# Performance work log

Measured on AMD Instinct MI355X. Metric: run time of the kernel, lower is better.

## Reference

```python
import jax, jax.numpy as jnp
import numpy as np

SOS_TOKEN = 1
MAX_LENGTH = 64
VOCAB = 32000
HIDDEN = 1024
BATCH = 32


def setup_inputs() -> dict:
    key = jax.random.key(0)
    ks = jax.random.split(key, 10)
    s = 1.0 / np.sqrt(HIDDEN)
    return {
        "encoder_outputs": jax.random.normal(ks[0], (BATCH, MAX_LENGTH, HIDDEN), dtype=jnp.float32),
        "encoder_hidden": jax.random.normal(ks[1], (1, BATCH, HIDDEN), dtype=jnp.float32),
        "target_tensor": jax.random.randint(ks[2], (BATCH, MAX_LENGTH), 0, VOCAB),
        "embedding": jax.random.normal(ks[3], (VOCAB, HIDDEN), dtype=jnp.float32),
        "W_ih": jax.random.uniform(ks[4], (3 * HIDDEN, HIDDEN), jnp.float32, -s, s),
        "W_hh": jax.random.uniform(ks[5], (3 * HIDDEN, HIDDEN), jnp.float32, -s, s),
        "b_ih": jax.random.uniform(ks[6], (3 * HIDDEN,), jnp.float32, -s, s),
        "b_hh": jax.random.uniform(ks[7], (3 * HIDDEN,), jnp.float32, -s, s),
        "out_W": jax.random.uniform(ks[8], (VOCAB, HIDDEN), jnp.float32, -s, s),
        "out_b": jax.random.uniform(ks[9], (VOCAB,), jnp.float32, -s, s),
    }


def _decode(encoder_hidden, target_tensor, embedding, W_ih, W_hh, b_ih, b_hh, out_W, out_b):
    B = target_tensor.shape[0]
    # teacher forcing: input at step i is SOS (i=0) else target[:, i-1]
    sos = jnp.full((B, 1), SOS_TOKEN, dtype=target_tensor.dtype)
    inputs = jnp.concatenate([sos, target_tensor[:, :-1]], axis=1)  # [B,T]
    x = jax.nn.relu(embedding[inputs])  # [B,T,H]
    # precompute all input-side gate projections in one GEMM: [B,T,3H]
    xg = jnp.einsum("bth,gh->btg", x, W_ih) + b_ih
    h0 = encoder_hidden[0]  # [B,H]

    def step(h, xg_t):
        hg = h @ W_hh.T + b_hh  # [B,3H]
        xr, xz, xn = jnp.split(xg_t, 3, axis=-1)
        hr, hz, hn = jnp.split(hg, 3, axis=-1)
        r = jax.nn.sigmoid(xr + hr)
        z = jax.nn.sigmoid(xz + hz)
        n = jnp.tanh(xn + r * hn)
        h_new = (1.0 - z) * n + z * h
        return h_new, h_new

    h_last, hs = jax.lax.scan(step, h0, jnp.swapaxes(xg, 0, 1))
    hs = jnp.swapaxes(hs, 0, 1)  # [B,T,H]
    logits = jnp.einsum("bth,vh->btv", hs, out_W) + out_b
    log_probs = jax.nn.log_softmax(logits, axis=-1)
    return log_probs, h_last[None]  # hidden shaped [1,B,H] like torch GRU


def reference(encoder_outputs, encoder_hidden, target_tensor, embedding, W_ih, W_hh, b_ih, b_hh, out_W, out_b):
    del encoder_outputs  # only used for batch size in the original
    return _decode(encoder_hidden, target_tensor, embedding, W_ih, W_hh, b_ih, b_hh, out_W, out_b)
```

## Files before the change

### kernel.cpp

```cpp
#include <hip/hip_runtime.h>
#include <hip/hip_bf16.h>

#define B_ 32
#define T_ 64
#define H_ 1024
#define G3 3072
#define V_ 32000
#define M_ 2048
#define NB_SCAN 64

typedef __attribute__((ext_vector_type(8))) short s16x8;
typedef __attribute__((ext_vector_type(4))) float f32x4;
typedef __bf16 bf16x8 __attribute__((ext_vector_type(8)));

__device__ inline unsigned short f2bf(float f) {
    union { float f; unsigned int u; } v; v.f = f;
    unsigned int u = v.u;
    return (unsigned short)((u + 0x7FFFu + ((u >> 16) & 1u)) >> 16);
}

__device__ inline s16x8 load_b128_cc(const void* p) {
    s16x8 r;
    asm volatile("global_load_dwordx4 %0, %1, off sc0 sc1" : "=v"(r) : "v"(p));
    return r;
}
__device__ inline unsigned int load_b32_cc(const void* p) {
    unsigned int r;
    asm volatile("global_load_dword %0, %1, off sc0 sc1" : "=v"(r) : "v"(p));
    return r;
}
__device__ inline void store_b32_cc(void* p, unsigned int v) {
    asm volatile("global_store_dword %0, %1, off sc0 sc1" :: "v"(p), "v"(v) : "memory");
}

__global__ void cast_f32_bf16(const float* __restrict__ src, unsigned short* __restrict__ dst, int n) {
    int i = (blockIdx.x * blockDim.x + threadIdx.x) * 4;
    int stride = gridDim.x * blockDim.x * 4;
    for (; i < n; i += stride) {
        float4 v = *(const float4*)(src + i);
        ushort4 o;
        o.x = f2bf(v.x); o.y = f2bf(v.y); o.z = f2bf(v.z); o.w = f2bf(v.w);
        *(ushort4*)(dst + i) = o;
    }
}

__global__ void embed_relu(const int* __restrict__ target, const float* __restrict__ emb,
                           unsigned short* __restrict__ x) {
    int m = blockIdx.x;
    int b = m >> 6, t = m & 63;
    int tok = (t == 0) ? 1 : target[b * T_ + t - 1];
    const float* row = emb + (size_t)tok * H_;
    int k = threadIdx.x * 4;
    float4 v = *(const float4*)(row + k);
    ushort4 o;
    o.x = f2bf(fmaxf(v.x, 0.f)); o.y = f2bf(fmaxf(v.y, 0.f));
    o.z = f2bf(fmaxf(v.z, 0.f)); o.w = f2bf(fmaxf(v.w, 0.f));
    *(ushort4*)(x + (size_t)m * H_ + k) = o;
}

__global__ void init_h(const float* __restrict__ enc_hidden, unsigned short* __restrict__ hb) {
    int i = blockIdx.x * blockDim.x + threadIdx.x;
    if (i < B_ * H_) hb[i] = f2bf(enc_hidden[i]);
}

__global__ void zero_u32(unsigned int* __restrict__ p, int n) {
    int i = blockIdx.x * blockDim.x + threadIdx.x;
    if (i < n) p[i] = 0;
}

__global__ __launch_bounds__(256) void gemm_bias(
    const unsigned short* __restrict__ A,
    const unsigned short* __restrict__ Bm,
    const float* __restrict__ bias,
    float* __restrict__ C,
    int N, int K)
{
    __shared__ __align__(16) unsigned short As[2 * 4096];
    __shared__ __align__(16) unsigned short Bs[2 * 4096];
    int n0 = blockIdx.x * 128, m0 = blockIdx.y * 128;
    int tid = threadIdx.x;
    int lane = tid & 63, wv = tid >> 6;
    int wr = wv >> 1, wc = wv & 1;

    f32x4 acc[4][4] = {};

    int o0 = wv * 2048 + lane * 16;
    int row0 = o0 >> 6, ib0 = (o0 & 63) >> 1;
    int o1 = o0 + 1024;
    int row1 = o1 >> 6, ib1 = (o1 & 63) >> 1;

    auto stage = [&](int buf, int k0) {
        const unsigned short* ga0 = A + (size_t)(m0 + row0) * K + k0 + ib0;
        const unsigned short* gb0 = Bm + (size_t)(n0 + row0) * K + k0 + ib0;
        const unsigned short* ga1 = A + (size_t)(m0 + row1) * K + k0 + ib1;
        const unsigned short* gb1 = Bm + (size_t)(n0 + row1) * K + k0 + ib1;
        unsigned short* la0 = As + buf * 4096 + wv * 1024;
        unsigned short* lb0 = Bs + buf * 4096 + wv * 1024;
        __builtin_amdgcn_global_load_lds((const __attribute__((address_space(1))) void*)ga0,
                                         (__attribute__((address_space(3))) void*)la0, 16, 0, 0);
        __builtin_amdgcn_global_load_lds((const __attribute__((address_space(1))) void*)gb0,
                                         (__attribute__((address_space(3))) void*)lb0, 16, 0, 0);
        __builtin_amdgcn_global_load_lds((const __attribute__((address_space(1))) void*)ga1,
                                         (__attribute__((address_space(3))) void*)(la0 + 512), 16, 0, 0);
        __builtin_amdgcn_global_load_lds((const __attribute__((address_space(1))) void*)gb1,
                                         (__attribute__((address_space(3))) void*)(lb0 + 512), 16, 0, 0);
    };

    int kq = (lane >> 4) * 8;
    int rA = wr * 64 + (lane & 15);
    int rB = wc * 64 + (lane & 15);

    int NT = K >> 5;
    stage(0, 0);
    __syncthreads();

    int cur = 0;
    for (int t = 0; t < NT; ++t) {
        if (t + 1 < NT) stage(cur ^ 1, (t + 1) << 5);
        const unsigned short* ab = As + cur * 4096;
        const unsigned short* bb = Bs + cur * 4096;
        s16x8 af[4], bf[4];
#pragma unroll
        for (int i = 0; i < 4; ++i) {
            af[i] = *(const s16x8*)(ab + (rA + i * 16) * 32 + kq);
            bf[i] = *(const s16x8*)(bb + (rB + i * 16) * 32 + kq);
        }
#pragma unroll
        for (int mf = 0; mf < 4; ++mf)
#pragma unroll
            for (int nf = 0; nf < 4; ++nf)
                acc[mf][nf] = __builtin_amdgcn_mfma_f32_16x16x32_bf16(
                    __builtin_bit_cast(bf16x8, af[mf]),
                    __builtin_bit_cast(bf16x8, bf[nf]),
                    acc[mf][nf], 0, 0, 0);
        __syncthreads();
        cur ^= 1;
    }

#pragma unroll
    for (int nf = 0; nf < 4; ++nf) {
        int col = n0 + wc * 64 + nf * 16 + (lane & 15);
        float bv = bias[col];
#pragma unroll
        for (int mf = 0; mf < 4; ++mf) {
            int mbase = m0 + wr * 64 + mf * 16 + (lane >> 4) * 4;
#pragma unroll
            for (int r = 0; r < 4; ++r)
                C[(size_t)(mbase + r) * N + col] = acc[mf][nf][r] + bv;
        }
    }
}

__global__ __launch_bounds__(256) void gru_scan(
    const unsigned short* __restrict__ Whhb,
    const float* __restrict__ b_hh,
    const float* __restrict__ enc_hidden,
    const float* __restrict__ xg,
    unsigned short* __restrict__ hb0, unsigned short* __restrict__ hb1,
    float* __restrict__ hfF,
    unsigned short* __restrict__ hs,
    unsigned int* __restrict__ flags)
{
    __shared__ __align__(16) unsigned short ws_[48 * 1024];
    __shared__ __align__(16) f32x4 red[2][3][64];

    int tid = threadIdx.x;
    int lane = tid & 63, wave = tid >> 6;
    int rt = wave >> 1, kh = wave & 1;
    int ct = blockIdx.x;

    for (int idx = tid; idx < 48 * 128; idx += 256) {
        int r = idx >> 7, slot = idx & 127;
        int g = r >> 4, jr = r & 15;
        s16x8 v = *(const s16x8*)(Whhb + (size_t)(g * H_ + ct * 16 + jr) * H_ + slot * 8);
        *(s16x8*)(ws_ + r * 1024 + (slot ^ (r & 7)) * 8) = v;
    }
    __syncthreads();

    int rr = lane & 15, q = lane >> 4;
    int col = ct * 16 + rr;
    int xsw = rr & 7;
    int kbase = kh * 512;
    int sbase = kh * 64 + q;
    float br = b_hh[col], bz = b_hh[H_ + col], bn = b_hh[2 * H_ + col];
    int b0 = rt * 16 + q * 4;

    float hold[4];
    if (kh == 1) {
#pragma unroll
        for (int r = 0; r < 4; ++r) hold[r] = enc_hidden[(b0 + r) * H_ + col];
    }

    for (int t = 0; t < T_; ++t) {
        const unsigned short* hbp = (t & 1) ? hb1 : hb0;
        unsigned short*       hbn = (t & 1) ? hb0 : hb1;

        const unsigned short* ha = hbp + (size_t)(rt * 16 + rr) * H_ + kbase + q * 8;
        s16x8 af[16];
#pragma unroll
        for (int i = 0; i < 16; ++i) af[i] = load_b128_cc(ha + i * 32);

        float xr[4], xz[4], xn[4];
        if (kh == 1) {
#pragma unroll
            for (int r = 0; r < 4; ++r) {
                const float* xrow = xg + ((size_t)(b0 + r) * T_ + t) * G3;
                xr[r] = xrow[col]; xz[r] = xrow[H_ + col]; xn[r] = xrow[2 * H_ + col];
            }
        }

        f32x4 accr, accz, accn;
        if (kh == 1) {
            accr = (f32x4){br, br, br, br};
            accz = (f32x4){bz, bz, bz, bz};
            accn = (f32x4){bn, bn, bn, bn};
        } else {
            accr = (f32x4){0.f, 0.f, 0.f, 0.f};
            accz = accr; accn = accr;
        }

        asm volatile("s_waitcnt vmcnt(0)");
        __builtin_amdgcn_sched_barrier(0);

#pragma unroll
        for (int kk = 0; kk < 16; ++kk) {
            int so = ((sbase + kk * 4) ^ xsw) * 8;
            s16x8 fr = *(const s16x8*)(ws_ + rr * 1024 + so);
            s16x8 fz = *(const s16x8*)(ws_ + (16 + rr) * 1024 + so);
            s16x8 fn = *(const s16x8*)(ws_ + (32 + rr) * 1024 + so);
            bf16x8 a = __builtin_bit_cast(bf16x8, af[kk]);
            accr = __builtin_amdgcn_mfma_f32_16x16x32_bf16(a, __builtin_bit_cast(bf16x8, fr), accr, 0, 0, 0);
            accz = __builtin_amdgcn_mfma_f32_16x16x32_bf16(a, __builtin_bit_cast(bf16x8, fz), accz, 0, 0, 0);
            accn = __builtin_amdgcn_mfma_f32_16x16x32_bf16(a, __builtin_bit_cast(bf16x8, fn), accn, 0, 0, 0);
        }

        if (kh == 0) {
            red[rt][0][lane] = accr; red[rt][1][lane] = accz; red[rt][2][lane] = accn;
        }
        __syncthreads();
        if (kh == 1) {
            accr += red[rt][0][lane]; accz += red[rt][1][lane]; accn += red[rt][2][lane];
            unsigned int hpk[4];
#pragma unroll
            for (int r = 0; r < 4; ++r) {
                float rg = 1.f / (1.f + __expf(-(xr[r] + accr[r])));
                float zg = 1.f / (1.f + __expf(-(xz[r] + accz[r])));
                float ng = tanhf(xn[r] + rg * accn[r]);
                float hnew = (1.f - zg) * ng + zg * hold[r];
                hold[r] = hnew;
                hpk[r] = f2bf(hnew);
            }
#pragma unroll
            for (int r = 0; r < 4; ++r) {
                unsigned int other = __shfl_xor((int)hpk[r], 1);
                if ((rr & 1) == 0) {
                    unsigned int pk = hpk[r] | (other << 16);
                    size_t e = (size_t)(b0 + r) * H_ + col;
                    store_b32_cc(hbn + e, pk);
                    *(unsigned int*)(hs + ((size_t)(b0 + r) * T_ + t) * H_ + col) = pk;
                }
            }
            if (t == T_ - 1) {
#pragma unroll
                for (int r = 0; r < 4; ++r) hfF[(b0 + r) * H_ + col] = hold[r];
            }
            asm volatile("s_waitcnt vmcnt(0)" ::: "memory");
        }

        if (t < T_ - 1) {
            __syncthreads();
            if (tid == 0) store_b32_cc(flags + ct, (unsigned int)(t + 1));
            unsigned int tgt = (unsigned int)(t + 1);
            while (true) {
                unsigned int f = load_b32_cc(flags + lane);
                asm volatile("s_waitcnt vmcnt(0)");
                if (__all(f >= tgt)) break;
                __builtin_amdgcn_s_sleep(1);
            }
            __builtin_amdgcn_sched_barrier(0);
        }
    }
}

__global__ __launch_bounds__(256) void log_softmax_inplace(float* __restrict__ out) {
    int m = blockIdx.x;
    float* row = out + (size_t)m * V_;
    int tid = threadIdx.x;
    __shared__ float sm[4], ss[4];

    float mx = -1e30f, s = 0.f;
    for (int i = tid * 4; i < V_; i += 1024) {
        float4 v = *(const float4*)(row + i);
        float lm = fmaxf(fmaxf(v.x, v.y), fmaxf(v.z, v.w));
        float ns = __expf(v.x - lm) + __expf(v.y - lm) + __expf(v.z - lm) + __expf(v.w - lm);
        if (lm > mx) { s = s * __expf(mx - lm) + ns; mx = lm; }
        else          { s += ns * __expf(lm - mx); }
    }
    for (int o = 32; o > 0; o >>= 1) {
        float om = __shfl_xor(mx, o), os = __shfl_xor(s, o);
        float nm = fmaxf(mx, om);
        s = s * __expf(mx - nm) + os * __expf(om - nm);
        mx = nm;
    }
    int wv = tid >> 6, lane = tid & 63;
    if (lane == 0) { sm[wv] = mx; ss[wv] = s; }
    __syncthreads();
    float fm = fmaxf(fmaxf(sm[0], sm[1]), fmaxf(sm[2], sm[3]));
    float fs = ss[0] * __expf(sm[0] - fm) + ss[1] * __expf(sm[1] - fm)
             + ss[2] * __expf(sm[2] - fm) + ss[3] * __expf(sm[3] - fm);
    float lse = fm + __logf(fs);

    for (int i = tid * 4; i < V_; i += 1024) {
        float4 v = *(const float4*)(row + i);
        v.x -= lse; v.y -= lse; v.z -= lse; v.w -= lse;
        *(float4*)(row + i) = v;
    }
}

__global__ void copy_f32(const float* __restrict__ src, float* __restrict__ dst, int n) {
    int i = blockIdx.x * blockDim.x + threadIdx.x;
    if (i < n) dst[i] = src[i];
}

extern "C" void kernel_launch(void* const* d_in, const int* in_sizes, int n_in,
                              void* d_out, int out_size, void* d_ws, size_t ws_size,
                              hipStream_t stream) {
    const float* enc_hidden = (const float*)d_in[1];
    const int*   target     = (const int*)d_in[2];
    const float* embedding  = (const float*)d_in[3];
    const float* W_ih       = (const float*)d_in[4];
    const float* W_hh       = (const float*)d_in[5];
    const float* b_ih       = (const float*)d_in[6];
    const float* b_hh       = (const float*)d_in[7];
    const float* out_W      = (const float*)d_in[8];
    const float* out_b      = (const float*)d_in[9];
    float* out = (float*)d_out;

    char* ws = (char*)d_ws;
    float*          xg   = (float*)(ws);
    unsigned short* xb   = (unsigned short*)(ws + 25165824);
    unsigned short* hsb  = (unsigned short*)(ws + 29360128);
    unsigned short* wihb = (unsigned short*)(ws + 33554432);
    unsigned short* whhb = (unsigned short*)(ws + 39845888);
    unsigned short* owb  = (unsigned short*)(ws + 46137344);
    float*          hfF  = (float*)(ws + 111673344);
    unsigned short* hb0  = (unsigned short*)(ws + 111804416);
    unsigned short* hb1  = (unsigned short*)(ws + 111869952);
    unsigned int*   flg  = (unsigned int*)(ws + 111935488);

    cast_f32_bf16<<<512, 256, 0, stream>>>(W_ih, wihb, G3 * H_);
    cast_f32_bf16<<<512, 256, 0, stream>>>(W_hh, whhb, G3 * H_);
    cast_f32_bf16<<<2048, 256, 0, stream>>>(out_W, owb, V_ * H_);
    embed_relu<<<M_, 256, 0, stream>>>(target, embedding, xb);
    init_h<<<128, 256, 0, stream>>>(enc_hidden, hb0);
    zero_u32<<<1, 64, 0, stream>>>(flg, 64);

    gemm_bias<<<dim3(G3 / 128, M_ / 128), 256, 0, stream>>>(xb, wihb, b_ih, xg, G3, H_);

    {
        void* args[] = { (void*)&whhb, (void*)&b_hh, (void*)&enc_hidden, (void*)&xg,
                         (void*)&hb0, (void*)&hb1, (void*)&hfF, (void*)&hsb, (void*)&flg };
        hipLaunchCooperativeKernel((const void*)gru_scan, dim3(NB_SCAN), dim3(256), args, 0, stream);
    }

    gemm_bias<<<dim3(V_ / 128, M_ / 128), 256, 0, stream>>>(hsb, owb, out_b, out, V_, H_);
    log_softmax_inplace<<<M_, 256, 0, stream>>>(out);
    copy_f32<<<128, 256, 0, stream>>>(hfF, out + (size_t)M_ * V_, B_ * H_);
}
```

Baseline: 936.9 us.

## Fuse per-tile softmax stats into logits GEMM epilogue and prefetch GRU inputs

The logits GEMM now computes per-row max and sum-exp for each 128-column tile in its epilogue and writes these partials to workspace. A lighter lse_sub kernel combines the 250 partials per row and subtracts the LSE, which removes one full read pass over the 2048x32000 logits. Separately, the GRU scan now loads the next step's xg gate inputs before the inter-block barrier spin, so that load latency overlaps the wait. The cost is extra epilogue shuffles and exp work in the GEMM, and the partials reuse the workspace region that held xb.

```diff
diff --git a/kernel.cpp b/kernel.cpp
--- a/kernel.cpp
+++ b/kernel.cpp
@@ -8,6 +8,7 @@
 #define V_ 32000
 #define M_ 2048
 #define NB_SCAN 64
+#define NTILE_N 250
 
 typedef __attribute__((ext_vector_type(8))) short s16x8;
 typedef __attribute__((ext_vector_type(4))) float f32x4;
@@ -151,6 +152,128 @@
     }
 }
 
+__global__ __launch_bounds__(256) void gemm_logits(
+    const unsigned short* __restrict__ A,
+    const unsigned short* __restrict__ Bm,
+    const float* __restrict__ bias,
+    float* __restrict__ C,
+    float* __restrict__ pmax,
+    float* __restrict__ psum)
+{
+    __shared__ __align__(16) unsigned short As[2 * 4096];
+    __shared__ __align__(16) unsigned short Bs[2 * 4096];
+    __shared__ float spx[2][128], sps[2][128];
+    int n0 = blockIdx.x * 128, m0 = blockIdx.y * 128;
+    int tid = threadIdx.x;
+    int lane = tid & 63, wv = tid >> 6;
+    int wr = wv >> 1, wc = wv & 1;
+
+    f32x4 acc[4][4] = {};
+
+    int o0 = wv * 2048 + lane * 16;
+    int row0 = o0 >> 6, ib0 = (o0 & 63) >> 1;
+    int o1 = o0 + 1024;
+    int row1 = o1 >> 6, ib1 = (o1 & 63) >> 1;
+
+    auto stage = [&](int buf, int k0) {
+        const unsigned short* ga0 = A + (size_t)(m0 + row0) * H_ + k0 + ib0;
+        const unsigned short* gb0 = Bm + (size_t)(n0 + row0) * H_ + k0 + ib0;
+        const unsigned short* ga1 = A + (size_t)(m0 + row1) * H_ + k0 + ib1;
+        const unsigned short* gb1 = Bm + (size_t)(n0 + row1) * H_ + k0 + ib1;
+        unsigned short* la0 = As + buf * 4096 + wv * 1024;
+        unsigned short* lb0 = Bs + buf * 4096 + wv * 1024;
+        __builtin_amdgcn_global_load_lds((const __attribute__((address_space(1))) void*)ga0,
+                                         (__attribute__((address_space(3))) void*)la0, 16, 0, 0);
+        __builtin_amdgcn_global_load_lds((const __attribute__((address_space(1))) void*)gb0,
+                                         (__attribute__((address_space(3))) void*)lb0, 16, 0, 0);
+        __builtin_amdgcn_global_load_lds((const __attribute__((address_space(1))) void*)ga1,
+                                         (__attribute__((address_space(3))) void*)(la0 + 512), 16, 0, 0);
+        __builtin_amdgcn_global_load_lds((const __attribute__((address_space(1))) void*)gb1,
+                                         (__attribute__((address_space(3))) void*)(lb0 + 512), 16, 0, 0);
+    };
+
+    int q = lane >> 4, rr2 = lane & 15;
+    int kq = q * 8;
+    int rA = wr * 64 + rr2;
+    int rB = wc * 64 + rr2;
+
+    stage(0, 0);
+    __syncthreads();
+
+    int cur = 0;
+    for (int t = 0; t < 32; ++t) {
+        if (t + 1 < 32) stage(cur ^ 1, (t + 1) << 5);
+        const unsigned short* ab = As + cur * 4096;
+        const unsigned short* bb = Bs + cur * 4096;
+        s16x8 af[4], bf[4];
+#pragma unroll
+        for (int i = 0; i < 4; ++i) {
+            af[i] = *(const s16x8*)(ab + (rA + i * 16) * 32 + kq);
+            bf[i] = *(const s16x8*)(bb + (rB + i * 16) * 32 + kq);
+        }
+#pragma unroll
+        for (int mf = 0; mf < 4; ++mf)
+#pragma unroll
+            for (int nf = 0; nf < 4; ++nf)
+                acc[mf][nf] = __builtin_amdgcn_mfma_f32_16x16x32_bf16(
+                    __builtin_bit_cast(bf16x8, af[mf]),
+                    __builtin_bit_cast(bf16x8, bf[nf]),
+                    acc[mf][nf], 0, 0, 0);
+        __syncthreads();
+        cur ^= 1;
+    }
+
+    float bv[4];
+#pragma unroll
+    for (int nf = 0; nf < 4; ++nf) bv[nf] = bias[n0 + wc * 64 + nf * 16 + rr2];
+
+#pragma unroll
+    for (int mf = 0; mf < 4; ++mf) {
+#pragma unroll
+        for (int r = 0; r < 4; ++r) {
+            int row_local = wr * 64 + mf * 16 + q * 4 + r;
+            float vmax = -1e30f;
+#pragma unroll
+            for (int nf = 0; nf < 4; ++nf) vmax = fmaxf(vmax, acc[mf][nf][r] + bv[nf]);
+#pragma unroll
+            for (int o = 1; o < 16; o <<= 1) vmax = fmaxf(vmax, __shfl_xor(vmax, o));
+            float vsum = 0.f;
+#pragma unroll
+            for (int nf = 0; nf < 4; ++nf) vsum += __expf(acc[mf][nf][r] + bv[nf] - vmax);
+#pragma unroll
+            for (int o = 1; o < 16; o <<= 1) vsum += __shfl_xor(vsum, o);
+            if (rr2 == 0) { spx[wc][row_local] = vmax; sps[wc][row_local] = vsum; }
+        }
+    }
+
+#pragma unroll
+    for (int nf = 0; nf < 4; ++nf) {
+        int col = n0 + wc * 64 + nf * 16 + rr2;
+#pragma unroll
+        for (int mf = 0; mf < 4; ++mf) {
+            int mbase = m0 + wr * 64 + mf * 16 + q * 4;
+#pragma unroll
+            for (int r = 0; r < 4; ++r)
+                C[(size_t)(mbase + r) * V_ + col] = acc[mf][nf][r] + bv[nf];
+        }
+    }
+
+    __syncthreads();
+    if (wc == 0 && rr2 == 0) {
+#pragma unroll
+        for (int mf = 0; mf < 4; ++mf)
+#pragma unroll
+            for (int r = 0; r < 4; ++r) {
+                int row_local = wr * 64 + mf * 16 + q * 4 + r;
+                float m0v = spx[0][row_local], m1v = spx[1][row_local];
+                float Mv = fmaxf(m0v, m1v);
+                float Sv = sps[0][row_local] * __expf(m0v - Mv) + sps[1][row_local] * __expf(m1v - Mv);
+                pmax[(size_t)(m0 + row_local) * NTILE_N + blockIdx.x] = Mv;
+                psum[(size_t)(m0 + row_local) * NTILE_N + blockIdx.x] = Sv;
+            }
+    }
+}
+
 __global__ __launch_bounds__(256) void gru_scan(
     const unsigned short* __restrict__ Whhb,
     const float* __restrict__ b_hh,
@@ -186,9 +309,14 @@
     int b0 = rt * 16 + q * 4;
 
     float hold[4];
+    float xr[4], xz[4], xn[4];
     if (kh == 1) {
 #pragma unroll
-        for (int r = 0; r < 4; ++r) hold[r] = enc_hidden[(b0 + r) * H_ + col];
+        for (int r = 0; r < 4; ++r) {
+            hold[r] = enc_hidden[(b0 + r) * H_ + col];
+            const float* xrow = xg + ((size_t)(b0 + r) * T_) * G3;
+            xr[r] = xrow[col]; xz[r] = xrow[H_ + col]; xn[r] = xrow[2 * H_ + col];
+        }
     }
 
     for (int t = 0; t < T_; ++t) {
@@ -199,15 +327,6 @@
         s16x8 af[16];
 #pragma unroll
         for (int i = 0; i < 16; ++i) af[i] = load_b128_cc(ha + i * 32);
-
-        float xr[4], xz[4], xn[4];
-        if (kh == 1) {
-#pragma unroll
-            for (int r = 0; r < 4; ++r) {
-                const float* xrow = xg + ((size_t)(b0 + r) * T_ + t) * G3;
-                xr[r] = xrow[col]; xz[r] = xrow[H_ + col]; xn[r] = xrow[2 * H_ + col];
-            }
-        }
 
         f32x4 accr, accz, accn;
         if (kh == 1) {
@@ -255,8 +374,7 @@
                 unsigned int other = __shfl_xor((int)hpk[r], 1);
                 if ((rr & 1) == 0) {
                     unsigned int pk = hpk[r] | (other << 16);
-                    size_t e = (size_t)(b0 + r) * H_ + col;
-                    store_b32_cc(hbn + e, pk);
+                    store_b32_cc(hbn + (size_t)(b0 + r) * H_ + col, pk);
                     *(unsigned int*)(hs + ((size_t)(b0 + r) * T_ + t) * H_ + col) = pk;
                 }
             }
@@ -270,6 +388,14 @@
         if (t < T_ - 1) {
             __syncthreads();
             if (tid == 0) store_b32_cc(flags + ct, (unsigned int)(t + 1));
+            if (kh == 1) {
+#pragma unroll
+                for (int r = 0; r < 4; ++r) {
+                    const float* xrow = xg + ((size_t)(b0 + r) * T_ + (t + 1)) * G3;
+                    xr[r] = xrow[col]; xz[r] = xrow[H_ + col]; xn[r] = xrow[2 * H_ + col];
+                }
+                __builtin_amdgcn_sched_barrier(0);
+            }
             unsigned int tgt = (unsigned int)(t + 1);
             while (true) {
                 unsigned int f = load_b32_cc(flags + lane);
@@ -282,34 +408,37 @@
     }
 }
 
-__global__ __launch_bounds__(256) void log_softmax_inplace(float* __restrict__ out) {
+__global__ __launch_bounds__(256) void lse_sub(
+    float* __restrict__ out,
+    const float* __restrict__ pmax, const float* __restrict__ psum)
+{
     int m = blockIdx.x;
-    float* row = out + (size_t)m * V_;
     int tid = threadIdx.x;
-    __shared__ float sm[4], ss[4];
-
-    float mx = -1e30f, s = 0.f;
-    for (int i = tid * 4; i < V_; i += 1024) {
-        float4 v = *(const float4*)(row + i);
-        float lm = fmaxf(fmaxf(v.x, v.y), fmaxf(v.z, v.w));
-        float ns = __expf(v.x - lm) + __expf(v.y - lm) + __expf(v.z - lm) + __expf(v.w - lm);
-        if (lm > mx) { s = s * __expf(mx - lm) + ns; mx = lm; }
-        else          { s += ns * __expf(lm - mx); }
+    __shared__ float sm[4], ssum[4];
+
+    float M = -1e30f, S = 0.f;
+    for (int i = tid; i < NTILE_N; i += 256) {
+        float pm_ = pmax[(size_t)m * NTILE_N + i];
+        float ps_ = psum[(size_t)m * NTILE_N + i];
+        float nm = fmaxf(M, pm_);
+        S = S * __expf(M - nm) + ps_ * __expf(pm_ - nm);
+        M = nm;
     }
     for (int o = 32; o > 0; o >>= 1) {
-        float om = __shfl_xor(mx, o), os = __shfl_xor(s, o);
-        float nm = fmaxf(mx, om);
-        s = s * __expf(mx - nm) + os * __expf(om - nm);
-        mx = nm;
+        float om = __shfl_xor(M, o), os = __shfl_xor(S, o);
+        float nm = fmaxf(M, om);
+        S = S * __expf(M - nm) + os * __expf(om - nm);
+        M = nm;
     }
     int wv = tid >> 6, lane = tid & 63;
-    if (lane == 0) { sm[wv] = mx; ss[wv] = s; }
+    if (lane == 0) { sm[wv] = M; ssum[wv] = S; }
     __syncthreads();
     float fm = fmaxf(fmaxf(sm[0], sm[1]), fmaxf(sm[2], sm[3]));
-    float fs = ss[0] * __expf(sm[0] - fm) + ss[1] * __expf(sm[1] - fm)
-             + ss[2] * __expf(sm[2] - fm) + ss[3] * __expf(sm[3] - fm);
+    float fs = ssum[0] * __expf(sm[0] - fm) + ssum[1] * __expf(sm[1] - fm)
+             + ssum[2] * __expf(sm[2] - fm) + ssum[3] * __expf(sm[3] - fm);
     float lse = fm + __logf(fs);
 
+    float* row = out + (size_t)m * V_;
     for (int i = tid * 4; i < V_; i += 1024) {
         float4 v = *(const float4*)(row + i);
         v.x -= lse; v.y -= lse; v.z -= lse; v.w -= lse;
@@ -347,6 +476,8 @@
     unsigned short* hb0  = (unsigned short*)(ws + 111804416);
     unsigned short* hb1  = (unsigned short*)(ws + 111869952);
     unsigned int*   flg  = (unsigned int*)(ws + 111935488);
+    float*          pmx  = (float*)(ws + 25165824);
+    float*          psm  = (float*)(ws + 25165824 + 2048000);
 
     cast_f32_bf16<<<512, 256, 0, stream>>>(W_ih, wihb, G3 * H_);
     cast_f32_bf16<<<512, 256, 0, stream>>>(W_hh, whhb, G3 * H_);
@@ -363,7 +494,7 @@
         hipLaunchCooperativeKernel((const void*)gru_scan, dim3(NB_SCAN), dim3(256), args, 0, stream);
     }
 
-    gemm_bias<<<dim3(V_ / 128, M_ / 128), 256, 0, stream>>>(hsb, owb, out_b, out, V_, H_);
-    log_softmax_inplace<<<M_, 256, 0, stream>>>(out);
+    gemm_logits<<<dim3(NTILE_N, M_ / 128), 256, 0, stream>>>(hsb, owb, out_b, out, pmx, psm);
+    lse_sub<<<M_, 256, 0, stream>>>(out, pmx, psm);
     copy_f32<<<128, 256, 0, stream>>>(hfF, out + (size_t)M_ * V_, B_ * H_);
 }
```

Result: faster. 904.0 us (-3.5%).
